# Optimization experiments

Measured on AMD Instinct MI355X. Metric: run time of the kernel, lower is better.

The kernel has to match this reference:

```python
import jax, jax.numpy as jnp
import numpy as np

NUM_ANCHORS = 3
MAX_DETECTIONS = 10
CONF_THRESH = 0.5


def setup_inputs() -> dict:
    key = jax.random.key(0)
    k1, k2, k3 = jax.random.split(key, 3)
    B, T, D = 32, 512, 2048
    features = jax.random.normal(k1, (B, T, D), dtype=jnp.float32)
    W_bbox = jax.random.normal(k2, (D, NUM_ANCHORS * 4), dtype=jnp.float32) * 0.02
    b_bbox = jnp.zeros((NUM_ANCHORS * 4,), dtype=jnp.float32)
    W_conf = jax.random.normal(k3, (D, NUM_ANCHORS), dtype=jnp.float32) * 0.02
    b_conf = jnp.zeros((NUM_ANCHORS,), dtype=jnp.float32)
    return {"features": features, "W_bbox": W_bbox, "b_bbox": b_bbox,
            "W_conf": W_conf, "b_conf": b_conf}


def reference(features, W_bbox, b_bbox, W_conf, b_conf):
    # features: [B, T, D]
    B, T, D = features.shape
    A = NUM_ANCHORS
    k = min(MAX_DETECTIONS, A)  # = 3

    # Dual linear heads (the two trivial GEMMs)
    bbox_pred = (jnp.einsum('btd,df->btf', features, W_bbox) + b_bbox).reshape(B, T, A, 4)
    conf_pred = jax.nn.sigmoid(jnp.einsum('btd,da->bta', features, W_conf) + b_conf)  # [B,T,A]

    # Vectorized replacement of the per-(b,t) Python loop:
    # top-k over anchors, gather boxes, threshold mask -> padded output.
    topk_conf, topk_idx = jax.lax.top_k(conf_pred, k)                    # [B,T,k]
    topk_boxes = jnp.take_along_axis(bbox_pred, topk_idx[..., None], axis=2)  # [B,T,k,4]
    valid = topk_conf > CONF_THRESH                                      # [B,T,k]
    # Invalid slots zeroed: matches the original's "drop invalid / zeros fallback"
    # semantics in a fixed-shape padded representation.
    boxes_out = jnp.where(valid[..., None], topk_boxes, 0.0)
    return boxes_out, topk_conf, valid
```

## Files before the change

kernel.cpp:

```cpp
#include <hip/hip_runtime.h>
#include <math.h>
#include <stdint.h>


#define DCOLS 2048
#define RPB   64
#define NW    16
#define CCH   64
#define NCH   (DCOLS / CCH)
#define NBUF  4
#define TILEF (RPB * CCH)
#define PSTR  15

__global__ __launch_bounds__(1024, 4)
void ped_det_kernel(const float* __restrict__ feat,
                    const float* __restrict__ Wb,
                    const float* __restrict__ bb,
                    const float* __restrict__ Wc,
                    const float* __restrict__ bc,
                    float* __restrict__ out,
                    int nrows)
{
    __shared__ __align__(16) float lds[NBUF][TILEF];
    float* P = &lds[0][0];
    float* S = P;

    const int t    = threadIdx.x;
    const int lane = t & 63;
    const int w    = t >> 6;
    const int wu   = __builtin_amdgcn_readfirstlane(w);

    const int rowBase = blockIdx.x * RPB;

    const int rsub = lane >> 4;
    const int su   = lane & 15;
    const int rst  = wu * 4 + rsub;
    const size_t gofs = (size_t)rst * DCOLS + ((su ^ (rst & 7)) << 2);
    const float* fbase = feat + (size_t)rowBase * DCOLS;

    auto STAGE = [&](int c, int p) {
        const float* g = fbase + gofs + c * CCH;
        const float* l = &lds[p][wu * 4 * CCH];
        __builtin_amdgcn_global_load_lds(
            (const __attribute__((address_space(1))) void*)g,
            (__attribute__((address_space(3))) void*)l, 16, 0, 0);
    };

    const int roff = lane * CCH + ((wu ^ (lane & 7)) << 2);

    float acc[15];
#pragma unroll
    for (int j = 0; j < 15; ++j) acc[j] = 0.0f;

    STAGE(0, 0);
    STAGE(1, 1);
    STAGE(2, 2);

    for (int c = 0; c < NCH; ++c) {
        if (c + 3 < NCH) STAGE(c + 3, (c + 3) & (NBUF - 1));

        const int rem = NCH - 1 - c;
        if (rem >= 3)      asm volatile("s_waitcnt vmcnt(3)" ::: "memory");
        else if (rem == 2) asm volatile("s_waitcnt vmcnt(2)" ::: "memory");
        else if (rem == 1) asm volatile("s_waitcnt vmcnt(1)" ::: "memory");
        else               asm volatile("s_waitcnt vmcnt(0)" ::: "memory");
        asm volatile("s_barrier" ::: "memory");

        const float* buf = &lds[c & (NBUF - 1)][0];
        const float4 f = *(const float4*)(buf + roff);

        const int du = c * CCH + wu * 4;
        const float* __restrict__ wbp = Wb + (size_t)du * 12;
        const float* __restrict__ wcp = Wc + (size_t)du * 3;
        const float fv[4] = { f.x, f.y, f.z, f.w };
#pragma unroll
        for (int j = 0; j < 4; ++j) {
            const float v = fv[j];
            acc[0]  += v * wbp[j * 12 + 0];
            acc[1]  += v * wbp[j * 12 + 1];
            acc[2]  += v * wbp[j * 12 + 2];
            acc[3]  += v * wbp[j * 12 + 3];
            acc[4]  += v * wbp[j * 12 + 4];
            acc[5]  += v * wbp[j * 12 + 5];
            acc[6]  += v * wbp[j * 12 + 6];
            acc[7]  += v * wbp[j * 12 + 7];
            acc[8]  += v * wbp[j * 12 + 8];
            acc[9]  += v * wbp[j * 12 + 9];
            acc[10] += v * wbp[j * 12 + 10];
            acc[11] += v * wbp[j * 12 + 11];
            acc[12] += v * wcp[j * 3 + 0];
            acc[13] += v * wcp[j * 3 + 1];
            acc[14] += v * wcp[j * 3 + 2];
        }

        asm volatile("s_waitcnt lgkmcnt(0)" ::: "memory");
        asm volatile("s_barrier" ::: "memory");
    }

    {
        float* pp = &P[(wu * RPB + lane) * PSTR];
#pragma unroll
        for (int j = 0; j < 15; ++j) pp[j] = acc[j];
    }
    __syncthreads();

    float sval = 0.0f;
    int rl = 0, jj = 0;
    if (t < RPB * 15) {
        rl = t / 15;
        jj = t % 15;
        float s = 0.0f;
#pragma unroll
        for (int w2 = 0; w2 < NW; ++w2)
            s += P[(w2 * RPB + rl) * PSTR + jj];
        s += (jj < 12) ? bb[jj] : bc[jj - 12];
        sval = s;
    }
    __syncthreads();

    if (t < RPB * 15)
        S[rl * 16 + jj] = sval;
    __syncthreads();

    if (t < RPB) {
        const int r2 = t;
        float box[12];
#pragma unroll
        for (int j = 0; j < 12; ++j) box[j] = S[r2 * 16 + j];
        float conf[3];
#pragma unroll
        for (int a = 0; a < 3; ++a)
            conf[a] = 1.0f / (1.0f + __expf(-S[r2 * 16 + 12 + a]));

        int i0 = 0; float m0 = conf[0];
        if (conf[1] > m0) { i0 = 1; m0 = conf[1]; }
        if (conf[2] > m0) { i0 = 2; m0 = conf[2]; }
        const int ra = (i0 == 0) ? 1 : 0;
        const int rb = (i0 == 2) ? 1 : 2;
        int i1, i2;
        if (conf[rb] > conf[ra]) { i1 = rb; i2 = ra; }
        else                     { i1 = ra; i2 = rb; }
        const int idx[3] = { i0, i1, i2 };

        const int ro = blockIdx.x * RPB + r2;
        float* boxout  = out + (size_t)ro * 12;
        float* confout = out + (size_t)nrows * 12 + (size_t)ro * 3;
        float* valout  = out + (size_t)nrows * 15 + (size_t)ro * 3;
#pragma unroll
        for (int sl = 0; sl < 3; ++sl) {
            const int   a   = idx[sl];
            const float cv  = conf[a];
            const bool  vld = cv > 0.5f;
            float4 bx;
            bx.x = vld ? box[a * 4 + 0] : 0.0f;
            bx.y = vld ? box[a * 4 + 1] : 0.0f;
            bx.z = vld ? box[a * 4 + 2] : 0.0f;
            bx.w = vld ? box[a * 4 + 3] : 0.0f;
            *(float4*)(boxout + sl * 4) = bx;
            confout[sl] = cv;
            valout[sl]  = vld ? 1.0f : 0.0f;
        }
    }
}

extern "C" void kernel_launch(void* const* d_in, const int* in_sizes, int n_in,
                              void* d_out, int out_size, void* d_ws, size_t ws_size,
                              hipStream_t stream) {
    const float* feat = (const float*)d_in[0];
    const float* Wb   = (const float*)d_in[1];
    const float* bb   = (const float*)d_in[2];
    const float* Wc   = (const float*)d_in[3];
    const float* bc   = (const float*)d_in[4];
    float* out = (float*)d_out;

    const int nrows   = in_sizes[0] / DCOLS;
    const int nblocks = nrows / RPB;

    ped_det_kernel<<<dim3(nblocks), dim3(1024), 0, stream>>>(
        feat, Wb, bb, Wc, bc, out, nrows);
}
```

Measured before the change: 40.06 us.

## Halve rows per block and split outputs across half-waves with wider chunks

Each block now handles 32 rows instead of 64. The stage width grows to 256 columns, and the 4-deep LDS ring becomes a 2-buffer double buffer. Each wave's lanes are split into two halves that compute different subsets of the 15 outputs, which cuts per-thread accumulators and weight loads and doubles the block count for better CU coverage. The trade-off is shallower prefetch depth and divergent half-wave branches, and the launch_bounds occupancy hint is dropped.

```diff
diff --git a/kernel.cpp b/kernel.cpp
--- a/kernel.cpp
+++ b/kernel.cpp
@@ -4,15 +4,14 @@
 
 
 #define DCOLS 2048
-#define RPB   64
+#define RPB   32
 #define NW    16
-#define CCH   64
-#define NCH   (DCOLS / CCH)
-#define NBUF  4
-#define TILEF (RPB * CCH)
+#define SCW   256
+#define NSC   (DCOLS / SCW)
+#define TILEF (RPB * SCW)
 #define PSTR  15
 
-__global__ __launch_bounds__(1024, 4)
+__global__ __launch_bounds__(1024)
 void ped_det_kernel(const float* __restrict__ feat,
                     const float* __restrict__ Wb,
                     const float* __restrict__ bb,
@@ -21,7 +20,7 @@
                     float* __restrict__ out,
                     int nrows)
 {
-    __shared__ __align__(16) float lds[NBUF][TILEF];
+    __shared__ __align__(16) float lds[2][TILEF];
     float* P = &lds[0][0];
     float* S = P;
 
@@ -29,68 +28,85 @@
     const int lane = t & 63;
     const int w    = t >> 6;
     const int wu   = __builtin_amdgcn_readfirstlane(w);
+    const int row  = lane & 31;
+    const int half = lane >> 5;
 
     const int rowBase = blockIdx.x * RPB;
-
-    const int rsub = lane >> 4;
-    const int su   = lane & 15;
-    const int rst  = wu * 4 + rsub;
-    const size_t gofs = (size_t)rst * DCOLS + ((su ^ (rst & 7)) << 2);
     const float* fbase = feat + (size_t)rowBase * DCOLS;
 
-    auto STAGE = [&](int c, int p) {
-        const float* g = fbase + gofs + c * CCH;
-        const float* l = &lds[p][wu * 4 * CCH];
-        __builtin_amdgcn_global_load_lds(
-            (const __attribute__((address_space(1))) void*)g,
-            (__attribute__((address_space(3))) void*)l, 16, 0, 0);
+    auto STAGE = [&](int sc, int p) {
+#pragma unroll
+        for (int i = 0; i < 2; ++i) {
+            const int r = wu * 2 + i;
+            const float* g = fbase + (size_t)r * DCOLS + sc * SCW
+                           + ((lane ^ (r & 7)) << 2);
+            const float* l = &lds[p][r * SCW];
+            __builtin_amdgcn_global_load_lds(
+                (const __attribute__((address_space(1))) void*)g,
+                (__attribute__((address_space(3))) void*)l, 16, 0, 0);
+        }
     };
 
-    const int roff = lane * CCH + ((wu ^ (lane & 7)) << 2);
-
-    float acc[15];
-#pragma unroll
-    for (int j = 0; j < 15; ++j) acc[j] = 0.0f;
+    float acc[8];
+#pragma unroll
+    for (int j = 0; j < 8; ++j) acc[j] = 0.0f;
 
     STAGE(0, 0);
-    STAGE(1, 1);
-    STAGE(2, 2);
-
-    for (int c = 0; c < NCH; ++c) {
-        if (c + 3 < NCH) STAGE(c + 3, (c + 3) & (NBUF - 1));
-
-        const int rem = NCH - 1 - c;
-        if (rem >= 3)      asm volatile("s_waitcnt vmcnt(3)" ::: "memory");
-        else if (rem == 2) asm volatile("s_waitcnt vmcnt(2)" ::: "memory");
-        else if (rem == 1) asm volatile("s_waitcnt vmcnt(1)" ::: "memory");
-        else               asm volatile("s_waitcnt vmcnt(0)" ::: "memory");
+
+    for (int sc = 0; sc < NSC; ++sc) {
+        if (sc + 1 < NSC) {
+            STAGE(sc + 1, (sc + 1) & 1);
+            asm volatile("s_waitcnt vmcnt(2)" ::: "memory");
+        } else {
+            asm volatile("s_waitcnt vmcnt(0)" ::: "memory");
+        }
         asm volatile("s_barrier" ::: "memory");
 
-        const float* buf = &lds[c & (NBUF - 1)][0];
-        const float4 f = *(const float4*)(buf + roff);
-
-        const int du = c * CCH + wu * 4;
-        const float* __restrict__ wbp = Wb + (size_t)du * 12;
-        const float* __restrict__ wcp = Wc + (size_t)du * 3;
-        const float fv[4] = { f.x, f.y, f.z, f.w };
-#pragma unroll
-        for (int j = 0; j < 4; ++j) {
-            const float v = fv[j];
-            acc[0]  += v * wbp[j * 12 + 0];
-            acc[1]  += v * wbp[j * 12 + 1];
-            acc[2]  += v * wbp[j * 12 + 2];
-            acc[3]  += v * wbp[j * 12 + 3];
-            acc[4]  += v * wbp[j * 12 + 4];
-            acc[5]  += v * wbp[j * 12 + 5];
-            acc[6]  += v * wbp[j * 12 + 6];
-            acc[7]  += v * wbp[j * 12 + 7];
-            acc[8]  += v * wbp[j * 12 + 8];
-            acc[9]  += v * wbp[j * 12 + 9];
-            acc[10] += v * wbp[j * 12 + 10];
-            acc[11] += v * wbp[j * 12 + 11];
-            acc[12] += v * wcp[j * 3 + 0];
-            acc[13] += v * wcp[j * 3 + 1];
-            acc[14] += v * wcp[j * 3 + 2];
+        const float* buf = &lds[sc & 1][0];
+        if (half == 0) {
+#pragma unroll
+            for (int q = 0; q < 4; ++q) {
+                const int s = wu * 4 + q;
+                const float4 f = *(const float4*)(buf + row * SCW
+                                                  + ((s ^ (row & 7)) << 2));
+                const int du = sc * SCW + wu * 16 + q * 4;
+                const float* __restrict__ wbp = Wb + (size_t)du * 12;
+                const float fv[4] = { f.x, f.y, f.z, f.w };
+#pragma unroll
+                for (int jj = 0; jj < 4; ++jj) {
+                    const float v = fv[jj];
+                    acc[0] += v * wbp[jj * 12 + 0];
+                    acc[1] += v * wbp[jj * 12 + 1];
+                    acc[2] += v * wbp[jj * 12 + 2];
+                    acc[3] += v * wbp[jj * 12 + 3];
+                    acc[4] += v * wbp[jj * 12 + 4];
+                    acc[5] += v * wbp[jj * 12 + 5];
+                    acc[6] += v * wbp[jj * 12 + 6];
+                    acc[7] += v * wbp[jj * 12 + 7];
+                }
+            }
+        } else {
+#pragma unroll
+            for (int q = 0; q < 4; ++q) {
+                const int s = wu * 4 + q;
+                const float4 f = *(const float4*)(buf + row * SCW
+                                                  + ((s ^ (row & 7)) << 2));
+                const int du = sc * SCW + wu * 16 + q * 4;
+                const float* __restrict__ wbp = Wb + (size_t)du * 12;
+                const float* __restrict__ wcp = Wc + (size_t)du * 3;
+                const float fv[4] = { f.x, f.y, f.z, f.w };
+#pragma unroll
+                for (int jj = 0; jj < 4; ++jj) {
+                    const float v = fv[jj];
+                    acc[0] += v * wbp[jj * 12 + 8];
+                    acc[1] += v * wbp[jj * 12 + 9];
+                    acc[2] += v * wbp[jj * 12 + 10];
+                    acc[3] += v * wbp[jj * 12 + 11];
+                    acc[4] += v * wcp[jj * 3 + 0];
+                    acc[5] += v * wcp[jj * 3 + 1];
+                    acc[6] += v * wcp[jj * 3 + 2];
+                }
+            }
         }
 
         asm volatile("s_waitcnt lgkmcnt(0)" ::: "memory");
@@ -98,9 +114,14 @@
     }
 
     {
-        float* pp = &P[(wu * RPB + lane) * PSTR];
-#pragma unroll
-        for (int j = 0; j < 15; ++j) pp[j] = acc[j];
+        float* pp = &P[(wu * RPB + row) * PSTR + half * 8];
+        if (half == 0) {
+#pragma unroll
+            for (int j = 0; j < 8; ++j) pp[j] = acc[j];
+        } else {
+#pragma unroll
+            for (int j = 0; j < 7; ++j) pp[j] = acc[j];
+        }
     }
     __syncthreads();
 
@@ -108,7 +129,7 @@
     int rl = 0, jj = 0;
     if (t < RPB * 15) {
         rl = t / 15;
-        jj = t % 15;
+        jj = t - rl * 15;
         float s = 0.0f;
 #pragma unroll
         for (int w2 = 0; w2 < NW; ++w2)
```

Measured after the change: 76.21 us. +90.3%, slower.

## Add large-chunk double-buffered kernel with dynamic LDS and rotated-phase fallback

Applied to the files above, without the earlier changes.

Adds a new kernel that stages 256-column chunks into a 128 KB double buffer in dynamic shared memory. Each wave issues four 16-byte loads per chunk, so the kernel has fewer barriers and chunk iterations. The launcher requests the larger dynamic LDS size and falls back to the old 64-column kernel if the request fails. The fallback kernel now rotates its starting chunk per block to spread accesses to the weight arrays. The 128 KB per block limits occupancy to one block per CU and shortens the prefetch depth from three chunks to one.

```diff
diff --git a/kernel.cpp b/kernel.cpp
--- a/kernel.cpp
+++ b/kernel.cpp
@@ -6,23 +6,23 @@
 #define DCOLS 2048
 #define RPB   64
 #define NW    16
-#define CCH   64
-#define NCH   (DCOLS / CCH)
-#define NBUF  4
-#define TILEF (RPB * CCH)
 #define PSTR  15
 
+#define CCH9  256
+#define NCH9  (DCOLS / CCH9)
+#define TILE9 (RPB * CCH9)
+
 __global__ __launch_bounds__(1024, 4)
-void ped_det_kernel(const float* __restrict__ feat,
-                    const float* __restrict__ Wb,
-                    const float* __restrict__ bb,
-                    const float* __restrict__ Wc,
-                    const float* __restrict__ bc,
-                    float* __restrict__ out,
-                    int nrows)
+void ped_det_kernel_dyn(const float* __restrict__ feat,
+                        const float* __restrict__ Wb,
+                        const float* __restrict__ bb,
+                        const float* __restrict__ Wc,
+                        const float* __restrict__ bc,
+                        float* __restrict__ out,
+                        int nrows)
 {
-    __shared__ __align__(16) float lds[NBUF][TILEF];
-    float* P = &lds[0][0];
+    extern __shared__ __align__(16) float lds[];
+    float* P = &lds[0];
     float* S = P;
 
     const int t    = threadIdx.x;
@@ -31,6 +31,162 @@
     const int wu   = __builtin_amdgcn_readfirstlane(w);
 
     const int rowBase = blockIdx.x * RPB;
+    const float* fbase = feat + (size_t)rowBase * DCOLS;
+
+    auto STAGE = [&](int c, int p) {
+#pragma unroll
+        for (int i = 0; i < 4; ++i) {
+            const int r = wu * 4 + i;
+            const float* g = fbase + (size_t)r * DCOLS + c * CCH9
+                           + ((lane ^ (r & 7)) << 2);
+            const float* l = &lds[(size_t)p * TILE9 + r * CCH9];
+            __builtin_amdgcn_global_load_lds(
+                (const __attribute__((address_space(1))) void*)g,
+                (__attribute__((address_space(3))) void*)l, 16, 0, 0);
+        }
+    };
+
+    float acc[15];
+#pragma unroll
+    for (int j = 0; j < 15; ++j) acc[j] = 0.0f;
+
+    STAGE(0, 0);
+
+    for (int c = 0; c < NCH9; ++c) {
+        if (c + 1 < NCH9) {
+            STAGE(c + 1, (c + 1) & 1);
+            asm volatile("s_waitcnt vmcnt(4)" ::: "memory");
+        } else {
+            asm volatile("s_waitcnt vmcnt(0)" ::: "memory");
+        }
+        asm volatile("s_barrier" ::: "memory");
+
+        const float* buf = &lds[(size_t)(c & 1) * TILE9];
+#pragma unroll
+        for (int q = 0; q < 4; ++q) {
+            const int s = wu * 4 + q;
+            const float4 f = *(const float4*)(buf + (size_t)lane * CCH9
+                                              + ((s ^ (lane & 7)) << 2));
+            const int du = c * CCH9 + wu * 16 + q * 4;
+            const float* __restrict__ wbp = Wb + (size_t)du * 12;
+            const float* __restrict__ wcp = Wc + (size_t)du * 3;
+            const float fv[4] = { f.x, f.y, f.z, f.w };
+#pragma unroll
+            for (int jj = 0; jj < 4; ++jj) {
+                const float v = fv[jj];
+                acc[0]  += v * wbp[jj * 12 + 0];
+                acc[1]  += v * wbp[jj * 12 + 1];
+                acc[2]  += v * wbp[jj * 12 + 2];
+                acc[3]  += v * wbp[jj * 12 + 3];
+                acc[4]  += v * wbp[jj * 12 + 4];
+                acc[5]  += v * wbp[jj * 12 + 5];
+                acc[6]  += v * wbp[jj * 12 + 6];
+                acc[7]  += v * wbp[jj * 12 + 7];
+                acc[8]  += v * wbp[jj * 12 + 8];
+                acc[9]  += v * wbp[jj * 12 + 9];
+                acc[10] += v * wbp[jj * 12 + 10];
+                acc[11] += v * wbp[jj * 12 + 11];
+                acc[12] += v * wcp[jj * 3 + 0];
+                acc[13] += v * wcp[jj * 3 + 1];
+                acc[14] += v * wcp[jj * 3 + 2];
+            }
+        }
+
+        asm volatile("s_waitcnt lgkmcnt(0)" ::: "memory");
+        asm volatile("s_barrier" ::: "memory");
+    }
+
+    {
+        float* pp = &P[(wu * RPB + lane) * PSTR];
+#pragma unroll
+        for (int j = 0; j < 15; ++j) pp[j] = acc[j];
+    }
+    __syncthreads();
+
+    float sval = 0.0f;
+    int rl = 0, jj = 0;
+    if (t < RPB * 15) {
+        rl = t / 15;
+        jj = t % 15;
+        float s = 0.0f;
+#pragma unroll
+        for (int w2 = 0; w2 < NW; ++w2)
+            s += P[(w2 * RPB + rl) * PSTR + jj];
+        s += (jj < 12) ? bb[jj] : bc[jj - 12];
+        sval = s;
+    }
+    __syncthreads();
+
+    if (t < RPB * 15)
+        S[rl * 16 + jj] = sval;
+    __syncthreads();
+
+    if (t < RPB) {
+        const int r2 = t;
+        float box[12];
+#pragma unroll
+        for (int j = 0; j < 12; ++j) box[j] = S[r2 * 16 + j];
+        float conf[3];
+#pragma unroll
+        for (int a = 0; a < 3; ++a)
+            conf[a] = 1.0f / (1.0f + __expf(-S[r2 * 16 + 12 + a]));
+
+        int i0 = 0; float m0 = conf[0];
+        if (conf[1] > m0) { i0 = 1; m0 = conf[1]; }
+        if (conf[2] > m0) { i0 = 2; m0 = conf[2]; }
+        const int ra = (i0 == 0) ? 1 : 0;
+        const int rb = (i0 == 2) ? 1 : 2;
+        int i1, i2;
+        if (conf[rb] > conf[ra]) { i1 = rb; i2 = ra; }
+        else                     { i1 = ra; i2 = rb; }
+        const int idx[3] = { i0, i1, i2 };
+
+        const int ro = blockIdx.x * RPB + r2;
+        float* boxout  = out + (size_t)ro * 12;
+        float* confout = out + (size_t)nrows * 12 + (size_t)ro * 3;
+        float* valout  = out + (size_t)nrows * 15 + (size_t)ro * 3;
+#pragma unroll
+        for (int sl = 0; sl < 3; ++sl) {
+            const int   a   = idx[sl];
+            const float cv  = conf[a];
+            const bool  vld = cv > 0.5f;
+            float4 bx;
+            bx.x = vld ? box[a * 4 + 0] : 0.0f;
+            bx.y = vld ? box[a * 4 + 1] : 0.0f;
+            bx.z = vld ? box[a * 4 + 2] : 0.0f;
+            bx.w = vld ? box[a * 4 + 3] : 0.0f;
+            *(float4*)(boxout + sl * 4) = bx;
+            confout[sl] = cv;
+            valout[sl]  = vld ? 1.0f : 0.0f;
+        }
+    }
+}
+
+#define CCH7  64
+#define NCH7  (DCOLS / CCH7)
+#define NBUF7 4
+#define TILE7 (RPB * CCH7)
+
+__global__ __launch_bounds__(1024, 4)
+void ped_det_kernel_64(const float* __restrict__ feat,
+                       const float* __restrict__ Wb,
+                       const float* __restrict__ bb,
+                       const float* __restrict__ Wc,
+                       const float* __restrict__ bc,
+                       float* __restrict__ out,
+                       int nrows)
+{
+    __shared__ __align__(16) float lds[NBUF7][TILE7];
+    float* P = &lds[0][0];
+    float* S = P;
+
+    const int t    = threadIdx.x;
+    const int lane = t & 63;
+    const int w    = t >> 6;
+    const int wu   = __builtin_amdgcn_readfirstlane(w);
+
+    const int rowBase = blockIdx.x * RPB;
+    const int bph = (int)(blockIdx.x) & (NCH7 - 1);
 
     const int rsub = lane >> 4;
     const int su   = lane & 15;
@@ -39,14 +195,15 @@
     const float* fbase = feat + (size_t)rowBase * DCOLS;
 
     auto STAGE = [&](int c, int p) {
-        const float* g = fbase + gofs + c * CCH;
-        const float* l = &lds[p][wu * 4 * CCH];
+        const int ca = (c + bph) & (NCH7 - 1);
+        const float* g = fbase + gofs + ca * CCH7;
+        const float* l = &lds[p][wu * 4 * CCH7];
         __builtin_amdgcn_global_load_lds(
             (const __attribute__((address_space(1))) void*)g,
             (__attribute__((address_space(3))) void*)l, 16, 0, 0);
     };
 
-    const int roff = lane * CCH + ((wu ^ (lane & 7)) << 2);
+    const int roff = lane * CCH7 + ((wu ^ (lane & 7)) << 2);
 
     float acc[15];
 #pragma unroll
@@ -56,20 +213,21 @@
     STAGE(1, 1);
     STAGE(2, 2);
 
-    for (int c = 0; c < NCH; ++c) {
-        if (c + 3 < NCH) STAGE(c + 3, (c + 3) & (NBUF - 1));
-
-        const int rem = NCH - 1 - c;
+    for (int c = 0; c < NCH7; ++c) {
+        if (c + 3 < NCH7) STAGE(c + 3, (c + 3) & (NBUF7 - 1));
+
+        const int rem = NCH7 - 1 - c;
         if (rem >= 3)      asm volatile("s_waitcnt vmcnt(3)" ::: "memory");
         else if (rem == 2) asm volatile("s_waitcnt vmcnt(2)" ::: "memory");
         else if (rem == 1) asm volatile("s_waitcnt vmcnt(1)" ::: "memory");
         else               asm volatile("s_waitcnt vmcnt(0)" ::: "memory");
         asm volatile("s_barrier" ::: "memory");
 
-        const float* buf = &lds[c & (NBUF - 1)][0];
+        const float* buf = &lds[c & (NBUF7 - 1)][0];
         const float4 f = *(const float4*)(buf + roff);
 
-        const int du = c * CCH + wu * 4;
+        const int ca = (c + bph) & (NCH7 - 1);
+        const int du = ca * CCH7 + wu * 4;
         const float* __restrict__ wbp = Wb + (size_t)du * 12;
         const float* __restrict__ wcp = Wc + (size_t)du * 3;
         const float fv[4] = { f.x, f.y, f.z, f.w };
@@ -176,6 +334,19 @@
     const int nrows   = in_sizes[0] / DCOLS;
     const int nblocks = nrows / RPB;
 
-    ped_det_kernel<<<dim3(nblocks), dim3(1024), 0, stream>>>(
-        feat, Wb, bb, Wc, bc, out, nrows);
+    static int dyn_ok = -1;
+    if (dyn_ok < 0) {
+        hipError_t e = hipFuncSetAttribute(
+            (const void*)ped_det_kernel_dyn,
+            hipFuncAttributeMaxDynamicSharedMemorySize, 2 * TILE9 * 4);
+        dyn_ok = (e == hipSuccess) ? 1 : 0;
+    }
+
+    if (dyn_ok == 1) {
+        ped_det_kernel_dyn<<<dim3(nblocks), dim3(1024), 2 * TILE9 * 4, stream>>>(
+            feat, Wb, bb, Wc, bc, out, nrows);
+    } else {
+        ped_det_kernel_64<<<dim3(nblocks), dim3(1024), 0, stream>>>(
+            feat, Wb, bb, Wc, bc, out, nrows);
+    }
 }
```

New measurement: 41.11 us. 2.6% more time.
